# Kernel tuning notes

Hardware: AMD Instinct MI355X
Metric: run time of the kernel (lower is better)

## Reference

```python
import jax, jax.numpy as jnp
import numpy as np

D_MODEL, HEAD, B, S = 1024, 64, 4, 2048

def setup_inputs() -> dict:
    key = jax.random.key(0)
    ks = jax.random.split(key, 7)
    sc = 0.02
    return {
        "x": jax.random.normal(ks[0], (B, S, D_MODEL), dtype=jnp.float32),
        "w_q": jax.random.normal(ks[1], (D_MODEL, HEAD), dtype=jnp.float32) * sc,
        "b_q": jax.random.normal(ks[2], (HEAD,), dtype=jnp.float32) * sc,
        "w_k": jax.random.normal(ks[3], (D_MODEL, HEAD), dtype=jnp.float32) * sc,
        "b_k": jax.random.normal(ks[4], (HEAD,), dtype=jnp.float32) * sc,
        "w_v": jax.random.normal(ks[5], (D_MODEL, HEAD), dtype=jnp.float32) * sc,
        "b_v": jax.random.normal(ks[6], (HEAD,), dtype=jnp.float32) * sc,
    }

def reference(x, w_q, b_q, w_k, b_k, w_v, b_v):
    # q, k, v: [B, S, H]
    q = jnp.einsum('bsd,dh->bsh', x, w_q) + b_q
    k = jnp.einsum('bsd,dh->bsh', x, w_k) + b_k
    v = jnp.einsum('bsd,dh->bsh', x, w_v) + b_v
    head = k.shape[-1]
    # Source divides by (1/sqrt(d)) i.e. multiplies by sqrt(d) -- kept faithful.
    scores = jnp.einsum('bqh,bkh->bqk', q, k) * jnp.sqrt(jnp.float32(head))
    seq = x.shape[1]
    causal = jnp.tril(jnp.ones((seq, seq), dtype=bool))  # [S, S]
    scores = jnp.where(causal, scores, -jnp.inf)
    att = jax.nn.softmax(scores, axis=-1)
    # dropout is identity in eval / p=0
    return jnp.einsum('bqk,bkh->bqh', att, v)
```

## Files before the change

kernel.cpp:

```cpp
#include <hip/hip_runtime.h>
#include <math.h>

#define D_MODEL 1024
#define HEAD 64
#define BATCH 4
#define SEQ 2048
#define M_TOT (BATCH*SEQ)

typedef short short8 __attribute__((ext_vector_type(8)));
typedef float f32x4 __attribute__((ext_vector_type(4)));
typedef unsigned short ushort_t;

typedef const __attribute__((address_space(1))) char* gas_t;
typedef __attribute__((address_space(3))) char* las_t;
#define GLDS16(src, dst) __builtin_amdgcn_global_load_lds((gas_t)(const void*)(src), (las_t)(void*)(dst), 16, 0, 0)

__device__ __forceinline__ unsigned short f2bf(float x) {
    union { float f; unsigned u; } v; v.f = x;
    unsigned r = (v.u + 0x7FFFu + ((v.u >> 16) & 1u)) >> 16;
    return (unsigned short)r;
}
__device__ __forceinline__ unsigned short f2bf_trunc(float x) {
    union { float f; unsigned u; } v; v.f = x;
    return (unsigned short)(v.u >> 16);
}
__device__ __forceinline__ float bf2f(unsigned short h) {
    union { unsigned u; float f; } v; v.u = ((unsigned)h) << 16;
    return v.f;
}

__global__ __launch_bounds__(256) void wsplit_kernel(
    const float* __restrict__ wq, const float* __restrict__ wk,
    const float* __restrict__ wv,
    ushort_t* __restrict__ Wfhi, ushort_t* __restrict__ Wflo)
{
    int tid = blockIdx.x * 256 + threadIdx.x;
    int l = tid & 63;
    int c = l & 15, g = l >> 4;
    int rest = tid >> 6;
    int nt = rest % 12, ks = rest / 12;
    const float* W = (nt < 4) ? wq : ((nt < 8) ? wk : wv);
    int colm = ((nt & 3) * 16) + c;
    short8 hi, lo;
#pragma unroll
    for (int e = 0; e < 8; ++e) {
        float v = W[(size_t)(32 * ks + 8 * g + e) * HEAD + colm];
        unsigned short h = f2bf_trunc(v);
        hi[e] = (short)h;
        lo[e] = (short)f2bf(v - bf2f(h));
    }
    *(short8*)&Wfhi[(size_t)tid * 8] = hi;
    *(short8*)&Wflo[(size_t)tid * 8] = lo;
}

__global__ __launch_bounds__(256) void proj_kernel(
    const float* __restrict__ x,
    const ushort_t* __restrict__ Wfhi, const ushort_t* __restrict__ Wflo,
    const float* __restrict__ bq, const float* __restrict__ bk,
    const float* __restrict__ bv,
    ushort_t* __restrict__ Qhi, ushort_t* __restrict__ Qlo,
    float* __restrict__ Kw, ushort_t* __restrict__ Vt)
{
    __shared__ __align__(16) char pbuf[65536];

    const int t = threadIdx.x;
    const int w = t >> 6;
    const int l = t & 63;
    const int c = l & 15, g = l >> 4;
    const int m0 = blockIdx.x * 16;

    char* wbase = pbuf + w * 16384;

    f32x4 acc[3];
#pragma unroll
    for (int j = 0; j < 3; ++j) acc[j] = (f32x4)0.0f;

    const float* xsrc = &x[(size_t)(m0 + c) * D_MODEL + 8 * g];

#define STAGE(i)                                                              \
    do {                                                                      \
        char* sb = wbase + ((i) & 1) * 8192;                                  \
        const float* xa = xsrc + (i) * 32;                                    \
        GLDS16(xa, sb);                                                       \
        GLDS16(xa + 4, sb + 1024);                                            \
        _Pragma("unroll")                                                     \
        for (int j = 0; j < 3; ++j) {                                         \
            const size_t wo = ((size_t)(i) * 12 + 3 * w + j) * 512 + l * 8;   \
            GLDS16(&Wfhi[wo], sb + 2048 + j * 1024);                          \
            GLDS16(&Wflo[wo], sb + 5120 + j * 1024);                          \
        }                                                                     \
    } while (0)

    STAGE(0);
    STAGE(1);

#pragma unroll 1
    for (int i = 0; i < 32; ++i) {
        if (i < 31) asm volatile("s_waitcnt vmcnt(8)" ::: "memory");
        else        asm volatile("s_waitcnt vmcnt(0)" ::: "memory");
        __builtin_amdgcn_sched_barrier(0);
        char* sb = wbase + (i & 1) * 8192;
        float4 fa = *(const float4*)(sb + l * 16);
        float4 fb = *(const float4*)(sb + 1024 + l * 16);
        float xs8[8] = {fa.x, fa.y, fa.z, fa.w, fb.x, fb.y, fb.z, fb.w};
        short8 xh, xl;
#pragma unroll
        for (int e = 0; e < 8; ++e) {
            unsigned short h = f2bf_trunc(xs8[e]);
            xh[e] = (short)h;
            xl[e] = (short)f2bf(xs8[e] - bf2f(h));
        }
#pragma unroll
        for (int j = 0; j < 3; ++j) {
            short8 wh = *(const short8*)(sb + 2048 + j * 1024 + l * 16);
            short8 wl_ = *(const short8*)(sb + 5120 + j * 1024 + l * 16);
            acc[j] = __builtin_amdgcn_mfma_f32_16x16x32_bf16(xh, wh, acc[j], 0, 0, 0);
            acc[j] = __builtin_amdgcn_mfma_f32_16x16x32_bf16(xl, wh, acc[j], 0, 0, 0);
            acc[j] = __builtin_amdgcn_mfma_f32_16x16x32_bf16(xh, wl_, acc[j], 0, 0, 0);
        }
        if (i < 30) STAGE(i + 2);
    }

    float* eldw = (float*)wbase;
#define ELD(j, r, cc) eldw[((j) * 16 + (r)) * 17 + (cc)]
#pragma unroll
    for (int j = 0; j < 3; ++j)
#pragma unroll
        for (int r = 0; r < 4; ++r)
            ELD(j, 4 * g + r, c) = acc[j][r];

    const int b = m0 >> 11;
    const int s0 = m0 & 2047;

#pragma unroll
    for (int j = 0; j < 3; ++j) {
        const int nt = 3 * w + j;
        const int col16 = (nt & 3) * 16;
        if (nt < 4) {
            const int row = l >> 2, cc4 = (l & 3) * 4;
            unsigned hu[2] = {0, 0}, lu[2] = {0, 0};
#pragma unroll
            for (int i = 0; i < 4; ++i) {
                float v = (ELD(j, row, cc4 + i) + bq[col16 + cc4 + i]) * 8.0f;
                unsigned short h = f2bf_trunc(v);
                unsigned short lo2 = f2bf(v - bf2f(h));
                hu[i >> 1] |= ((unsigned)h) << ((i & 1) * 16);
                lu[i >> 1] |= ((unsigned)lo2) << ((i & 1) * 16);
            }
            size_t off = (size_t)(m0 + row) * HEAD + col16 + cc4;
            *(uint2*)&Qhi[off] = make_uint2(hu[0], hu[1]);
            *(uint2*)&Qlo[off] = make_uint2(lu[0], lu[1]);
        } else if (nt < 8) {
            const int row = l >> 2, cc4 = (l & 3) * 4;
            float4 o;
            o.x = ELD(j, row, cc4 + 0) + bk[col16 + cc4 + 0];
            o.y = ELD(j, row, cc4 + 1) + bk[col16 + cc4 + 1];
            o.z = ELD(j, row, cc4 + 2) + bk[col16 + cc4 + 2];
            o.w = ELD(j, row, cc4 + 3) + bk[col16 + cc4 + 3];
            *(float4*)&Kw[(size_t)(m0 + row) * HEAD + col16 + cc4] = o;
        } else {
            const int dl = l >> 2, sg = (l & 3) * 4;
            const float bb = bv[col16 + dl];
            unsigned vu[2] = {0, 0};
#pragma unroll
            for (int i = 0; i < 4; ++i) {
                unsigned short v = f2bf(ELD(j, sg + i, dl) + bb);
                vu[i >> 1] |= ((unsigned)v) << ((i & 1) * 16);
            }
            *(uint2*)&Vt[((size_t)b * HEAD + col16 + dl) * SEQ + s0 + sg] =
                make_uint2(vu[0], vu[1]);
        }
    }
#undef ELD
#undef STAGE
}

#define NW 4
#define CHUNK 16
#define PSTR 72
#define NSEG 4

__global__ __launch_bounds__(256) void attn_part_kernel(
    const ushort_t* __restrict__ Qhi, const ushort_t* __restrict__ Qlo,
    const float* __restrict__ Kw, const ushort_t* __restrict__ Vt,
    float* __restrict__ Pm_ws, float* __restrict__ Pl_ws,
    float* __restrict__ Po_ws)
{
    __shared__ float Po[NW][CHUNK][68];
    __shared__ float Pm[NW][CHUNK];
    __shared__ float Pl[NW][CHUNK];
    __shared__ __align__(16) ushort_t Plds[NW][CHUNK][PSTR];

    const int t = threadIdx.x;
    const int w = t >> 6;
    const int l = t & 63;
    int id = blockIdx.x;
    int seg, base;
    if (id < 128)      { seg = 0; base = 0;   }
    else if (id < 224) { seg = 1; base = 128; }
    else if (id < 288) { seg = 2; base = 224; }
    else               { seg = 3; base = 288; }
    const int chunk = 127 - (id - base);
    const int b = blockIdx.y;
    const int q0 = chunk * CHUNK;

    const int c = l & 15;
    const int g = l >> 4;

    short8 qhi[2], qlo[2];
    {
        const ushort_t* qbase = &Qhi[(size_t)(b * SEQ + q0 + c) * HEAD];
        const ushort_t* qbasel = &Qlo[(size_t)(b * SEQ + q0 + c) * HEAD];
#pragma unroll
        for (int dc = 0; dc < 2; ++dc) {
            qhi[dc] = *(const short8*)&qbase[dc * 32 + 8 * g];
            qlo[dc] = *(const short8*)&qbasel[dc * 32 + 8 * g];
        }
    }

    f32x4 acc[4];
#pragma unroll
    for (int dt = 0; dt < 4; ++dt) acc[dt] = (f32x4)0.0f;
    float mrun = -1e30f, lsum = 0.f;

#pragma unroll 1
    for (int i = 0; i < 2; ++i) {
        const int tl = seg * 8 + w + 4 * i;
        const int c0 = tl * 64;
        if (c0 > q0 + CHUNK - 1) continue;

        int nlive = ((q0 + 15 - c0) >> 4) + 1;
        nlive = nlive > 4 ? 4 : nlive;

        float sc[4][4];
        float tmax = -1e30f;
#pragma unroll
        for (int t4 = 0; t4 < 4; ++t4) {
            if (t4 < nlive) {
                f32x4 st = (f32x4)0.0f;
#pragma unroll
                for (int dc = 0; dc < 2; ++dc) {
                    const float* kp = &Kw[(size_t)(b * SEQ + c0 + 16 * t4 + c) * HEAD + dc * 32 + 8 * g];
                    float4 a = *(const float4*)kp;
                    float4 b2 = *(const float4*)(kp + 4);
                    float ks8[8] = {a.x, a.y, a.z, a.w, b2.x, b2.y, b2.z, b2.w};
                    short8 khi, klo;
#pragma unroll
                    for (int e = 0; e < 8; ++e) {
                        unsigned short h = f2bf(ks8[e]);
                        khi[e] = (short)h;
                        klo[e] = (short)f2bf(ks8[e] - bf2f(h));
                    }
                    st = __builtin_amdgcn_mfma_f32_16x16x32_bf16(khi, qhi[dc], st, 0, 0, 0);
                    st = __builtin_amdgcn_mfma_f32_16x16x32_bf16(khi, qlo[dc], st, 0, 0, 0);
                    st = __builtin_amdgcn_mfma_f32_16x16x32_bf16(klo, qhi[dc], st, 0, 0, 0);
                }
#pragma unroll
                for (int r = 0; r < 4; ++r) {
                    int kv = c0 + 16 * t4 + 4 * g + r;
                    float s = (kv <= q0 + c) ? st[r] : -1e30f;
                    sc[t4][r] = s;
                    tmax = fmaxf(tmax, s);
                }
            } else {
#pragma unroll
                for (int r = 0; r < 4; ++r) sc[t4][r] = -1e30f;
            }
        }
        tmax = fmaxf(tmax, __shfl_xor(tmax, 16));
        tmax = fmaxf(tmax, __shfl_xor(tmax, 32));
        float newm = fmaxf(mrun, tmax);
        float corr = __expf(mrun - newm);
        mrun = newm;

        float psum = 0.f;
#pragma unroll
        for (int t4 = 0; t4 < 4; ++t4) {
            if (t4 < nlive) {
#pragma unroll
                for (int r = 0; r < 4; ++r) {
                    float pp = __expf(sc[t4][r] - newm);
                    sc[t4][r] = pp;
                    psum += pp;
                }
            } else {
#pragma unroll
                for (int r = 0; r < 4; ++r) sc[t4][r] = 0.f;
            }
        }
        psum += __shfl_xor(psum, 16);
        psum += __shfl_xor(psum, 32);
        lsum = lsum * corr + psum;

#pragma unroll
        for (int r = 0; r < 4; ++r) {
            float cq = __shfl(corr, 4 * g + r);
#pragma unroll
            for (int dt = 0; dt < 4; ++dt) acc[dt][r] *= cq;
        }

#pragma unroll
        for (int t4 = 0; t4 < 4; ++t4) {
            uint2 u;
            u.x = (unsigned)f2bf(sc[t4][0]) | ((unsigned)f2bf(sc[t4][1]) << 16);
            u.y = (unsigned)f2bf(sc[t4][2]) | ((unsigned)f2bf(sc[t4][3]) << 16);
            *(uint2*)&Plds[w][c][16 * t4 + 4 * g] = u;
        }
        const int nkvc = (nlive + 1) >> 1;
#pragma unroll
        for (int kvc = 0; kvc < 2; ++kvc) {
            if (kvc < nkvc) {
                short8 pf = *(short8*)&Plds[w][c][kvc * 32 + 8 * g];
#pragma unroll
                for (int dt = 0; dt < 4; ++dt) {
                    const ushort_t* vp =
                        &Vt[((size_t)(b * HEAD) + 16 * dt + c) * SEQ + c0 + kvc * 32 + 8 * g];
                    short8 vf = *(const short8*)vp;
                    acc[dt] = __builtin_amdgcn_mfma_f32_16x16x32_bf16(pf, vf, acc[dt], 0, 0, 0);
                }
            }
        }
    }

    if (g == 0) { Pm[w][c] = mrun; Pl[w][c] = lsum; }
#pragma unroll
    for (int dt = 0; dt < 4; ++dt)
#pragma unroll
        for (int r = 0; r < 4; ++r)
            Po[w][4 * g + r][16 * dt + c] = acc[dt][r];
    __syncthreads();

    const int mr = t >> 4;
    const int md = (t & 15) * 4;
    float M = Pm[0][mr];
#pragma unroll
    for (int ww = 1; ww < NW; ++ww) M = fmaxf(M, Pm[ww][mr]);
    float L = 0.f;
    float4 O; O.x = O.y = O.z = O.w = 0.f;
#pragma unroll
    for (int ww = 0; ww < NW; ++ww) {
        float f = __expf(Pm[ww][mr] - M);
        L += f * Pl[ww][mr];
        float4 p = *(const float4*)&Po[ww][mr][md];
        O.x += f * p.x; O.y += f * p.y; O.z += f * p.z; O.w += f * p.w;
    }
    const size_t part = ((size_t)(b * 128 + chunk)) * NSEG + seg;
    *(float4*)&Po_ws[(part * CHUNK + mr) * HEAD + md] = O;
    if ((t & 15) == 0) {
        Pm_ws[part * CHUNK + mr] = M;
        Pl_ws[part * CHUNK + mr] = L;
    }
}

__global__ __launch_bounds__(256) void attn_merge_kernel(
    const float* __restrict__ Pm_ws, const float* __restrict__ Pl_ws,
    const float* __restrict__ Po_ws, float* __restrict__ out)
{
    const int t = threadIdx.x;
    const int chunk = blockIdx.x;
    const int b = blockIdx.y;
    const int nparts = (chunk >> 5) + 1;
    const int mr = t >> 4;
    const int md = (t & 15) * 4;
    const size_t pbase = ((size_t)(b * 128 + chunk)) * NSEG;

    float M = -1e30f;
#pragma unroll 1
    for (int p = 0; p < nparts; ++p)
        M = fmaxf(M, Pm_ws[(pbase + p) * CHUNK + mr]);
    float L = 0.f;
    float4 O; O.x = O.y = O.z = O.w = 0.f;
#pragma unroll 1
    for (int p = 0; p < nparts; ++p) {
        float f = __expf(Pm_ws[(pbase + p) * CHUNK + mr] - M);
        L += f * Pl_ws[(pbase + p) * CHUNK + mr];
        float4 po = *(const float4*)&Po_ws[((pbase + p) * CHUNK + mr) * HEAD + md];
        O.x += f * po.x; O.y += f * po.y; O.z += f * po.z; O.w += f * po.w;
    }
    float inv = 1.0f / L;
    float4 res; res.x = O.x * inv; res.y = O.y * inv; res.z = O.z * inv; res.w = O.w * inv;
    *(float4*)&out[(size_t)(b * SEQ + chunk * CHUNK + mr) * HEAD + md] = res;
}

extern "C" void kernel_launch(void* const* d_in, const int* in_sizes, int n_in,
                              void* d_out, int out_size, void* d_ws, size_t ws_size,
                              hipStream_t stream) {
    (void)in_sizes; (void)n_in; (void)out_size; (void)ws_size;
    const float* x  = (const float*)d_in[0];
    const float* wq = (const float*)d_in[1];
    const float* bq = (const float*)d_in[2];
    const float* wk = (const float*)d_in[3];
    const float* bk = (const float*)d_in[4];
    const float* wv = (const float*)d_in[5];
    const float* bv = (const float*)d_in[6];
    float* out = (float*)d_out;

    ushort_t* Wfhi = (ushort_t*)d_ws;
    ushort_t* Wflo = Wfhi + (size_t)D_MODEL * 192;
    ushort_t* Qhi  = Wflo + (size_t)D_MODEL * 192;
    ushort_t* Qlo  = Qhi + (size_t)M_TOT * HEAD;
    float*    Kw   = (float*)(Qlo + (size_t)M_TOT * HEAD);
    ushort_t* Vt   = (ushort_t*)(Kw + (size_t)M_TOT * HEAD);
    float* Pm_ws = (float*)(Vt + (size_t)M_TOT * HEAD);
    float* Pl_ws = Pm_ws + (size_t)BATCH * 128 * NSEG * CHUNK;
    float* Po_ws = Pl_ws + (size_t)BATCH * 128 * NSEG * CHUNK;

    hipLaunchKernelGGL(wsplit_kernel, dim3(96), dim3(256), 0, stream,
                       wq, wk, wv, Wfhi, Wflo);
    hipLaunchKernelGGL(proj_kernel, dim3(M_TOT / 16), dim3(256), 0, stream,
                       x, Wfhi, Wflo, bq, bk, bv, Qhi, Qlo, Kw, Vt);
    hipLaunchKernelGGL(attn_part_kernel, dim3(320, BATCH), dim3(256),
                       0, stream, Qhi, Qlo, Kw, Vt, Pm_ws, Pl_ws, Po_ws);
    hipLaunchKernelGGL(attn_merge_kernel, dim3(SEQ / CHUNK, BATCH), dim3(256),
                       0, stream, Pm_ws, Pl_ws, Po_ws, out);
}
```

Baseline: 77.07 us.

## Split projection work per wave into column pairs and triple-buffer loads

The projection kernel now gives each wave an independent job: a 16-row tile paired with 2 of the 12 output column tiles, where before one block covered all 12 across its 4 waves. This yields 1.5x more blocks and less work per wave. Staging moves from double to triple buffering with adjusted vmcnt waits, to hide more global-load latency. The cost is that each x row tile is now loaded from global memory six times instead of once per block, and LDS per block grows.

```diff
diff --git a/kernel.cpp b/kernel.cpp
--- a/kernel.cpp
+++ b/kernel.cpp
@@ -61,45 +61,46 @@
     ushort_t* __restrict__ Qhi, ushort_t* __restrict__ Qlo,
     float* __restrict__ Kw, ushort_t* __restrict__ Vt)
 {
-    __shared__ __align__(16) char pbuf[65536];
+    __shared__ __align__(16) char pbuf[73728];
 
     const int t = threadIdx.x;
     const int w = t >> 6;
     const int l = t & 63;
     const int c = l & 15, g = l >> 4;
-    const int m0 = blockIdx.x * 16;
-
-    char* wbase = pbuf + w * 16384;
-
-    f32x4 acc[3];
-#pragma unroll
-    for (int j = 0; j < 3; ++j) acc[j] = (f32x4)0.0f;
-
+    const int job = blockIdx.x * 4 + w;
+    const int mt = job / 6;
+    const int pair = job - mt * 6;
+    const int m0 = mt * 16;
+
+    char* wbase = pbuf + w * 18432;
+
+    f32x4 acc0 = (f32x4)0.0f, acc1 = (f32x4)0.0f;
     const float* xsrc = &x[(size_t)(m0 + c) * D_MODEL + 8 * g];
 
 #define STAGE(i)                                                              \
     do {                                                                      \
-        char* sb = wbase + ((i) & 1) * 8192;                                  \
+        char* sb = wbase + ((i) % 3) * 6144;                                  \
         const float* xa = xsrc + (i) * 32;                                    \
         GLDS16(xa, sb);                                                       \
         GLDS16(xa + 4, sb + 1024);                                            \
-        _Pragma("unroll")                                                     \
-        for (int j = 0; j < 3; ++j) {                                         \
-            const size_t wo = ((size_t)(i) * 12 + 3 * w + j) * 512 + l * 8;   \
-            GLDS16(&Wfhi[wo], sb + 2048 + j * 1024);                          \
-            GLDS16(&Wflo[wo], sb + 5120 + j * 1024);                          \
-        }                                                                     \
+        const size_t wo0 = ((size_t)(i) * 12 + 2 * pair) * 512 + l * 8;       \
+        GLDS16(&Wfhi[wo0], sb + 2048);                                        \
+        GLDS16(&Wflo[wo0], sb + 3072);                                        \
+        GLDS16(&Wfhi[wo0 + 512], sb + 4096);                                  \
+        GLDS16(&Wflo[wo0 + 512], sb + 5120);                                  \
     } while (0)
 
     STAGE(0);
     STAGE(1);
+    STAGE(2);
 
 #pragma unroll 1
     for (int i = 0; i < 32; ++i) {
-        if (i < 31) asm volatile("s_waitcnt vmcnt(8)" ::: "memory");
-        else        asm volatile("s_waitcnt vmcnt(0)" ::: "memory");
+        if (i < 30)       asm volatile("s_waitcnt vmcnt(12)" ::: "memory");
+        else if (i == 30) asm volatile("s_waitcnt vmcnt(6)" ::: "memory");
+        else              asm volatile("s_waitcnt vmcnt(0)" ::: "memory");
         __builtin_amdgcn_sched_barrier(0);
-        char* sb = wbase + (i & 1) * 8192;
+        char* sb = wbase + (i % 3) * 6144;
         float4 fa = *(const float4*)(sb + l * 16);
         float4 fb = *(const float4*)(sb + 1024 + l * 16);
         float xs8[8] = {fa.x, fa.y, fa.z, fa.w, fb.x, fb.y, fb.z, fb.w};
@@ -110,31 +111,37 @@
             xh[e] = (short)h;
             xl[e] = (short)f2bf(xs8[e] - bf2f(h));
         }
-#pragma unroll
-        for (int j = 0; j < 3; ++j) {
-            short8 wh = *(const short8*)(sb + 2048 + j * 1024 + l * 16);
-            short8 wl_ = *(const short8*)(sb + 5120 + j * 1024 + l * 16);
-            acc[j] = __builtin_amdgcn_mfma_f32_16x16x32_bf16(xh, wh, acc[j], 0, 0, 0);
-            acc[j] = __builtin_amdgcn_mfma_f32_16x16x32_bf16(xl, wh, acc[j], 0, 0, 0);
-            acc[j] = __builtin_amdgcn_mfma_f32_16x16x32_bf16(xh, wl_, acc[j], 0, 0, 0);
-        }
-        if (i < 30) STAGE(i + 2);
-    }
+        short8 wh0 = *(const short8*)(sb + 2048 + l * 16);
+        short8 wl0 = *(const short8*)(sb + 3072 + l * 16);
+        short8 wh1 = *(const short8*)(sb + 4096 + l * 16);
+        short8 wl1 = *(const short8*)(sb + 5120 + l * 16);
+        acc0 = __builtin_amdgcn_mfma_f32_16x16x32_bf16(xh, wh0, acc0, 0, 0, 0);
+        acc0 = __builtin_amdgcn_mfma_f32_16x16x32_bf16(xl, wh0, acc0, 0, 0, 0);
+        acc0 = __builtin_amdgcn_mfma_f32_16x16x32_bf16(xh, wl0, acc0, 0, 0, 0);
+        acc1 = __builtin_amdgcn_mfma_f32_16x16x32_bf16(xh, wh1, acc1, 0, 0, 0);
+        acc1 = __builtin_amdgcn_mfma_f32_16x16x32_bf16(xl, wh1, acc1, 0, 0, 0);
+        acc1 = __builtin_amdgcn_mfma_f32_16x16x32_bf16(xh, wl1, acc1, 0, 0, 0);
+        if (i < 29) STAGE(i + 3);
+    }
+#undef STAGE
 
     float* eldw = (float*)wbase;
 #define ELD(j, r, cc) eldw[((j) * 16 + (r)) * 17 + (cc)]
-#pragma unroll
-    for (int j = 0; j < 3; ++j)
-#pragma unroll
-        for (int r = 0; r < 4; ++r)
-            ELD(j, 4 * g + r, c) = acc[j][r];
+    {
+        f32x4 a[2] = {acc0, acc1};
+#pragma unroll
+        for (int j = 0; j < 2; ++j)
+#pragma unroll
+            for (int r = 0; r < 4; ++r)
+                ELD(j, 4 * g + r, c) = a[j][r];
+    }
 
     const int b = m0 >> 11;
     const int s0 = m0 & 2047;
 
 #pragma unroll
-    for (int j = 0; j < 3; ++j) {
-        const int nt = 3 * w + j;
+    for (int j = 0; j < 2; ++j) {
+        const int nt = 2 * pair + j;
         const int col16 = (nt & 3) * 16;
         if (nt < 4) {
             const int row = l >> 2, cc4 = (l & 3) * 4;
@@ -172,7 +179,6 @@
         }
     }
 #undef ELD
-#undef STAGE
 }
 
 #define NW 4
@@ -407,7 +413,7 @@
 
     hipLaunchKernelGGL(wsplit_kernel, dim3(96), dim3(256), 0, stream,
                        wq, wk, wv, Wfhi, Wflo);
-    hipLaunchKernelGGL(proj_kernel, dim3(M_TOT / 16), dim3(256), 0, stream,
+    hipLaunchKernelGGL(proj_kernel, dim3(M_TOT / 16 * 6 / 4), dim3(256), 0, stream,
                        x, Wfhi, Wflo, bq, bk, bv, Qhi, Qlo, Kw, Vt);
     hipLaunchKernelGGL(attn_part_kernel, dim3(320, BATCH), dim3(256),
                        0, stream, Qhi, Qlo, Kw, Vt, Pm_ws, Pl_ws, Po_ws);
```

Result: slower. 99.47 us (+29.1%).

## Process 32 rows per projection block to reuse weight tiles twice

Applied to the files above, without the earlier changes.

The projection kernel now computes two 16-row subtiles per block and shares each staged weight hi/lo tile across both, so W is streamed from L2 half as often. LDS per block grows to 80KB and accumulators double. The grid is halved to 256 blocks, roughly one block per CU, which reduces the number of blocks available to hide latency.

```diff
diff --git a/kernel.cpp b/kernel.cpp
--- a/kernel.cpp
+++ b/kernel.cpp
@@ -61,33 +61,37 @@
     ushort_t* __restrict__ Qhi, ushort_t* __restrict__ Qlo,
     float* __restrict__ Kw, ushort_t* __restrict__ Vt)
 {
-    __shared__ __align__(16) char pbuf[65536];
+    __shared__ __align__(16) char pbuf[81920];
 
     const int t = threadIdx.x;
     const int w = t >> 6;
     const int l = t & 63;
     const int c = l & 15, g = l >> 4;
-    const int m0 = blockIdx.x * 16;
-
-    char* wbase = pbuf + w * 16384;
-
-    f32x4 acc[3];
-#pragma unroll
-    for (int j = 0; j < 3; ++j) acc[j] = (f32x4)0.0f;
-
-    const float* xsrc = &x[(size_t)(m0 + c) * D_MODEL + 8 * g];
+    const int m0 = blockIdx.x * 32;
+
+    char* wbase = pbuf + w * 20480;
+
+    f32x4 acc[3][2];
+#pragma unroll
+    for (int j = 0; j < 3; ++j)
+#pragma unroll
+        for (int s = 0; s < 2; ++s) acc[j][s] = (f32x4)0.0f;
+
+    const float* xsrc0 = &x[(size_t)(m0 + c) * D_MODEL + 8 * g];
+    const float* xsrc1 = &x[(size_t)(m0 + 16 + c) * D_MODEL + 8 * g];
 
 #define STAGE(i)                                                              \
     do {                                                                      \
-        char* sb = wbase + ((i) & 1) * 8192;                                  \
-        const float* xa = xsrc + (i) * 32;                                    \
-        GLDS16(xa, sb);                                                       \
-        GLDS16(xa + 4, sb + 1024);                                            \
+        char* sb = wbase + ((i) & 1) * 10240;                                 \
+        GLDS16(xsrc0 + (i) * 32, sb);                                         \
+        GLDS16(xsrc0 + (i) * 32 + 4, sb + 1024);                              \
+        GLDS16(xsrc1 + (i) * 32, sb + 2048);                                  \
+        GLDS16(xsrc1 + (i) * 32 + 4, sb + 3072);                              \
         _Pragma("unroll")                                                     \
         for (int j = 0; j < 3; ++j) {                                         \
             const size_t wo = ((size_t)(i) * 12 + 3 * w + j) * 512 + l * 8;   \
-            GLDS16(&Wfhi[wo], sb + 2048 + j * 1024);                          \
-            GLDS16(&Wflo[wo], sb + 5120 + j * 1024);                          \
+            GLDS16(&Wfhi[wo], sb + 4096 + j * 1024);                          \
+            GLDS16(&Wflo[wo], sb + 7168 + j * 1024);                          \
         }                                                                     \
     } while (0)
 
@@ -96,83 +100,93 @@
 
 #pragma unroll 1
     for (int i = 0; i < 32; ++i) {
-        if (i < 31) asm volatile("s_waitcnt vmcnt(8)" ::: "memory");
+        if (i < 31) asm volatile("s_waitcnt vmcnt(10)" ::: "memory");
         else        asm volatile("s_waitcnt vmcnt(0)" ::: "memory");
         __builtin_amdgcn_sched_barrier(0);
-        char* sb = wbase + (i & 1) * 8192;
-        float4 fa = *(const float4*)(sb + l * 16);
-        float4 fb = *(const float4*)(sb + 1024 + l * 16);
-        float xs8[8] = {fa.x, fa.y, fa.z, fa.w, fb.x, fb.y, fb.z, fb.w};
-        short8 xh, xl;
-#pragma unroll
-        for (int e = 0; e < 8; ++e) {
-            unsigned short h = f2bf_trunc(xs8[e]);
-            xh[e] = (short)h;
-            xl[e] = (short)f2bf(xs8[e] - bf2f(h));
+        char* sb = wbase + (i & 1) * 10240;
+        short8 xh[2], xl[2];
+#pragma unroll
+        for (int s = 0; s < 2; ++s) {
+            float4 fa = *(const float4*)(sb + s * 2048 + l * 16);
+            float4 fb = *(const float4*)(sb + s * 2048 + 1024 + l * 16);
+            float xs8[8] = {fa.x, fa.y, fa.z, fa.w, fb.x, fb.y, fb.z, fb.w};
+#pragma unroll
+            for (int e = 0; e < 8; ++e) {
+                unsigned short h = f2bf_trunc(xs8[e]);
+                xh[s][e] = (short)h;
+                xl[s][e] = (short)f2bf(xs8[e] - bf2f(h));
+            }
         }
 #pragma unroll
         for (int j = 0; j < 3; ++j) {
-            short8 wh = *(const short8*)(sb + 2048 + j * 1024 + l * 16);
-            short8 wl_ = *(const short8*)(sb + 5120 + j * 1024 + l * 16);
-            acc[j] = __builtin_amdgcn_mfma_f32_16x16x32_bf16(xh, wh, acc[j], 0, 0, 0);
-            acc[j] = __builtin_amdgcn_mfma_f32_16x16x32_bf16(xl, wh, acc[j], 0, 0, 0);
-            acc[j] = __builtin_amdgcn_mfma_f32_16x16x32_bf16(xh, wl_, acc[j], 0, 0, 0);
+            short8 wh = *(const short8*)(sb + 4096 + j * 1024 + l * 16);
+            short8 wl_ = *(const short8*)(sb + 7168 + j * 1024 + l * 16);
+#pragma unroll
+            for (int s = 0; s < 2; ++s) {
+                acc[j][s] = __builtin_amdgcn_mfma_f32_16x16x32_bf16(xh[s], wh, acc[j][s], 0, 0, 0);
+                acc[j][s] = __builtin_amdgcn_mfma_f32_16x16x32_bf16(xl[s], wh, acc[j][s], 0, 0, 0);
+                acc[j][s] = __builtin_amdgcn_mfma_f32_16x16x32_bf16(xh[s], wl_, acc[j][s], 0, 0, 0);
+            }
         }
         if (i < 30) STAGE(i + 2);
     }
+#undef STAGE
 
     float* eldw = (float*)wbase;
 #define ELD(j, r, cc) eldw[((j) * 16 + (r)) * 17 + (cc)]
-#pragma unroll
-    for (int j = 0; j < 3; ++j)
-#pragma unroll
-        for (int r = 0; r < 4; ++r)
-            ELD(j, 4 * g + r, c) = acc[j][r];
-
-    const int b = m0 >> 11;
-    const int s0 = m0 & 2047;
-
-#pragma unroll
-    for (int j = 0; j < 3; ++j) {
-        const int nt = 3 * w + j;
-        const int col16 = (nt & 3) * 16;
-        if (nt < 4) {
-            const int row = l >> 2, cc4 = (l & 3) * 4;
-            unsigned hu[2] = {0, 0}, lu[2] = {0, 0};
-#pragma unroll
-            for (int i = 0; i < 4; ++i) {
-                float v = (ELD(j, row, cc4 + i) + bq[col16 + cc4 + i]) * 8.0f;
-                unsigned short h = f2bf_trunc(v);
-                unsigned short lo2 = f2bf(v - bf2f(h));
-                hu[i >> 1] |= ((unsigned)h) << ((i & 1) * 16);
-                lu[i >> 1] |= ((unsigned)lo2) << ((i & 1) * 16);
-            }
-            size_t off = (size_t)(m0 + row) * HEAD + col16 + cc4;
-            *(uint2*)&Qhi[off] = make_uint2(hu[0], hu[1]);
-            *(uint2*)&Qlo[off] = make_uint2(lu[0], lu[1]);
-        } else if (nt < 8) {
-            const int row = l >> 2, cc4 = (l & 3) * 4;
-            float4 o;
-            o.x = ELD(j, row, cc4 + 0) + bk[col16 + cc4 + 0];
-            o.y = ELD(j, row, cc4 + 1) + bk[col16 + cc4 + 1];
-            o.z = ELD(j, row, cc4 + 2) + bk[col16 + cc4 + 2];
-            o.w = ELD(j, row, cc4 + 3) + bk[col16 + cc4 + 3];
-            *(float4*)&Kw[(size_t)(m0 + row) * HEAD + col16 + cc4] = o;
-        } else {
-            const int dl = l >> 2, sg = (l & 3) * 4;
-            const float bb = bv[col16 + dl];
-            unsigned vu[2] = {0, 0};
-#pragma unroll
-            for (int i = 0; i < 4; ++i) {
-                unsigned short v = f2bf(ELD(j, sg + i, dl) + bb);
-                vu[i >> 1] |= ((unsigned)v) << ((i & 1) * 16);
-            }
-            *(uint2*)&Vt[((size_t)b * HEAD + col16 + dl) * SEQ + s0 + sg] =
-                make_uint2(vu[0], vu[1]);
+#pragma unroll 1
+    for (int s = 0; s < 2; ++s) {
+        const int ms = m0 + 16 * s;
+#pragma unroll
+        for (int j = 0; j < 3; ++j)
+#pragma unroll
+            for (int r = 0; r < 4; ++r)
+                ELD(j, 4 * g + r, c) = acc[j][s][r];
+
+        const int b = ms >> 11;
+        const int s0 = ms & 2047;
+
+#pragma unroll
+        for (int j = 0; j < 3; ++j) {
+            const int nt = 3 * w + j;
+            const int col16 = (nt & 3) * 16;
+            if (nt < 4) {
+                const int row = l >> 2, cc4 = (l & 3) * 4;
+                unsigned hu[2] = {0, 0}, lu[2] = {0, 0};
+#pragma unroll
+                for (int i = 0; i < 4; ++i) {
+                    float v = (ELD(j, row, cc4 + i) + bq[col16 + cc4 + i]) * 8.0f;
+                    unsigned short h = f2bf_trunc(v);
+                    unsigned short lo2 = f2bf(v - bf2f(h));
+                    hu[i >> 1] |= ((unsigned)h) << ((i & 1) * 16);
+                    lu[i >> 1] |= ((unsigned)lo2) << ((i & 1) * 16);
+                }
+                size_t off = (size_t)(ms + row) * HEAD + col16 + cc4;
+                *(uint2*)&Qhi[off] = make_uint2(hu[0], hu[1]);
+                *(uint2*)&Qlo[off] = make_uint2(lu[0], lu[1]);
+            } else if (nt < 8) {
+                const int row = l >> 2, cc4 = (l & 3) * 4;
+                float4 o;
+                o.x = ELD(j, row, cc4 + 0) + bk[col16 + cc4 + 0];
+                o.y = ELD(j, row, cc4 + 1) + bk[col16 + cc4 + 1];
+                o.z = ELD(j, row, cc4 + 2) + bk[col16 + cc4 + 2];
+                o.w = ELD(j, row, cc4 + 3) + bk[col16 + cc4 + 3];
+                *(float4*)&Kw[(size_t)(ms + row) * HEAD + col16 + cc4] = o;
+            } else {
+                const int dl = l >> 2, sg = (l & 3) * 4;
+                const float bb = bv[col16 + dl];
+                unsigned vu[2] = {0, 0};
+#pragma unroll
+                for (int i = 0; i < 4; ++i) {
+                    unsigned short v = f2bf(ELD(j, sg + i, dl) + bb);
+                    vu[i >> 1] |= ((unsigned)v) << ((i & 1) * 16);
+                }
+                *(uint2*)&Vt[((size_t)b * HEAD + col16 + dl) * SEQ + s0 + sg] =
+                    make_uint2(vu[0], vu[1]);
+            }
         }
     }
 #undef ELD
-#undef STAGE
 }
 
 #define NW 4
@@ -407,7 +421,7 @@
 
     hipLaunchKernelGGL(wsplit_kernel, dim3(96), dim3(256), 0, stream,
                        wq, wk, wv, Wfhi, Wflo);
-    hipLaunchKernelGGL(proj_kernel, dim3(M_TOT / 16), dim3(256), 0, stream,
+    hipLaunchKernelGGL(proj_kernel, dim3(M_TOT / 32), dim3(256), 0, stream,
                        x, Wfhi, Wflo, bq, bk, bv, Qhi, Qlo, Kw, Vt);
     hipLaunchKernelGGL(attn_part_kernel, dim3(320, BATCH), dim3(256),
                        0, stream, Qhi, Qlo, Kw, Vt, Pm_ws, Pl_ws, Po_ws);
```

New measurement: 83.55 us. 1.08x slower.
